# Performance work log

Measured on AMD Instinct MI355X. Metric: run time of the kernel, lower is better.

## Reference

```python
import jax, jax.numpy as jnp
import numpy as np

K = 7
TOWERS = 4
X_SIZE = 8
POS_SIZE = 3
NUM_GRAPHS = 128
NODES_PER_GRAPH = 512
N = NUM_GRAPHS * NODES_PER_GRAPH
EPS_STD = 1e-5  # PyG StdAggregation eps
BN_EPS = 1e-5
# degree histogram passed to PNAConv.__init__ -> avg log-degree used by scalers
_DEG_HIST = np.array([0, 0, 0, 0, 0, 100, 200, 700], dtype=np.float64)
_BINS = np.arange(_DEG_HIST.shape[0], dtype=np.float64)
AVG_DEG_LOG = float((np.log(_BINS + 1.0) * _DEG_HIST).sum() / _DEG_HIST.sum())


def knn_graph(pos, num_graphs, k):
    # batched kNN (loop=False): each node gets its k nearest neighbors within its graph
    Nn, D = pos.shape
    n = Nn // num_graphs
    p = pos.reshape(num_graphs, n, D)
    d2 = jnp.sum((p[:, :, None, :] - p[:, None, :, :]) ** 2, axis=-1)  # [B,n,n]
    d2 = d2 + jnp.eye(n, dtype=d2.dtype) * 1e10  # exclude self-loops
    _, idx = jax.lax.top_k(-d2, k)  # [B,n,k] local neighbor ids
    offs = (jnp.arange(num_graphs) * n)[:, None, None]
    return (idx + offs).reshape(Nn, k)  # global source ids per target node


def pna_conv(x, nbr, W_pre, b_pre, W_post, b_post, W_lin, b_lin):
    # PyG PNAConv, towers=4, pre_layers=1, post_layers=1, divide_input=False, edge_dim=None
    Nn, F = x.shape
    k = nbr.shape[1]
    x_j = x[nbr]                                              # gather sources [N,k,F]
    x_i = jnp.broadcast_to(x[:, None, :], (Nn, k, F))         # target features
    h = jnp.concatenate([x_i, x_j], axis=-1)                  # [N,k,2F]
    m = jnp.einsum('nke,tef->nktf', h, W_pre) + b_pre         # per-tower pre-MLP [N,k,T,F]
    mean = m.mean(axis=1)
    mn = m.min(axis=1)
    mx = m.max(axis=1)
    var = jnp.mean(m * m, axis=1) - mean * mean               # PyG VarAggregation
    std = jnp.sqrt(jax.nn.relu(var) + EPS_STD)
    agg = jnp.concatenate([mean, mn, mx, std], axis=-1)       # [N,T,4F]
    amp = jnp.log(k + 1.0) / AVG_DEG_LOG                      # deg == k for every node in a knn graph
    scaled = jnp.concatenate([agg, agg * amp, agg * (1.0 / amp)], axis=-1)  # identity/amp/atten [N,T,12F]
    out = jnp.concatenate([jnp.broadcast_to(x[:, None, :], (Nn, TOWERS, F)), scaled], axis=-1)  # [N,T,13F]
    out = jnp.einsum('ntg,tgf->ntf', out, W_post) + b_post    # per-tower post-MLP [N,T,F_out]
    out = out.reshape(Nn, -1)
    return out @ W_lin + b_lin                                # mixing Linear(out,out)


def batch_norm(x, g, b):
    # training-mode BatchNorm1d over the node dimension
    mu = x.mean(axis=0)
    var = x.var(axis=0)
    return g * (x - mu) * jax.lax.rsqrt(var + BN_EPS) + b


def forward(x, pos, W_pre1, b_pre1, W_post1, b_post1, W_lin1, b_lin1, bn1_g, bn1_b,
            W_pre2, b_pre2, W_post2, b_post2, W_lin2, b_lin2, bn2_g, bn2_b, num_graphs):
    nbr = knn_graph(pos, num_graphs, K)
    h = jax.nn.relu(batch_norm(pna_conv(x, nbr, W_pre1, b_pre1, W_post1, b_post1, W_lin1, b_lin1), bn1_g, bn1_b))
    h = jax.nn.relu(batch_norm(pna_conv(h, nbr, W_pre2, b_pre2, W_post2, b_post2, W_lin2, b_lin2), bn2_g, bn2_b))
    return h.reshape(num_graphs, -1, h.shape[-1]).mean(axis=1)  # global mean pool -> [B,128]


def _winit(key, shape):
    fan_in = shape[-2]
    return (jax.random.normal(key, shape, dtype=jnp.float32) / jnp.sqrt(jnp.float32(fan_in))).astype(jnp.float32)


def setup_inputs() -> dict:
    key = jax.random.key(0)
    ks = jax.random.split(key, 8)
    F1, F2 = X_SIZE, 64
    return {
        'x': jax.random.normal(ks[0], (N, X_SIZE), dtype=jnp.float32),
        'pos': jax.random.normal(ks[1], (N, POS_SIZE), dtype=jnp.float32),
        'W_pre1': _winit(ks[2], (TOWERS, 2 * F1, F1)),
        'b_pre1': jnp.zeros((TOWERS, F1), jnp.float32),
        'W_post1': _winit(ks[3], (TOWERS, 13 * F1, 64 // TOWERS)),
        'b_post1': jnp.zeros((TOWERS, 64 // TOWERS), jnp.float32),
        'W_lin1': _winit(ks[4], (64, 64)),
        'b_lin1': jnp.zeros((64,), jnp.float32),
        'bn1_g': jnp.ones((64,), jnp.float32),
        'bn1_b': jnp.zeros((64,), jnp.float32),
        'W_pre2': _winit(ks[5], (TOWERS, 2 * F2, F2)),
        'b_pre2': jnp.zeros((TOWERS, F2), jnp.float32),
        'W_post2': _winit(ks[6], (TOWERS, 13 * F2, 128 // TOWERS)),
        'b_post2': jnp.zeros((TOWERS, 128 // TOWERS), jnp.float32),
        'W_lin2': _winit(ks[7], (128, 128)),
        'b_lin2': jnp.zeros((128,), jnp.float32),
        'bn2_g': jnp.ones((128,), jnp.float32),
        'bn2_b': jnp.zeros((128,), jnp.float32),
        'num_graphs': NUM_GRAPHS,
    }


def reference(x, pos, W_pre1, b_pre1, W_post1, b_post1, W_lin1, b_lin1, bn1_g, bn1_b,
              W_pre2, b_pre2, W_post2, b_post2, W_lin2, b_lin2, bn2_g, bn2_b, num_graphs):
    return forward(x, pos, W_pre1, b_pre1, W_post1, b_post1, W_lin1, b_lin1, bn1_g, bn1_b,
                   W_pre2, b_pre2, W_post2, b_post2, W_lin2, b_lin2, bn2_g, bn2_b, num_graphs)
```

## Files before the change

kernel.cpp:

```cpp
#include <hip/hip_runtime.h>
#include <math.h>


#define NGRAPH 128
#define NPG    512
#define NN     (NGRAPH*NPG)
#define KNB    7

constexpr double AVG_DEG_LOG_D = 2.0239670479173344;
constexpr double LOG8_D        = 2.0794415416798357;

typedef _Float16 f16x8 __attribute__((ext_vector_type(8)));
typedef _Float16 h2    __attribute__((ext_vector_type(2)));
typedef float    f32x4 __attribute__((ext_vector_type(4)));

__device__ __forceinline__ unsigned short f2h(float x) {
    _Float16 h = (_Float16)x;
    return __builtin_bit_cast(unsigned short, h);
}

__global__ __launch_bounds__(256) void prep_kernel(
    const float* __restrict__ Wpost1, const float* __restrict__ Wpost2,
    const float* __restrict__ Wpre2,  const float* __restrict__ Wlin2,
    const float* __restrict__ Wlin1,
    unsigned short* __restrict__ Wf1p, unsigned short* __restrict__ Wf1l,
    unsigned short* __restrict__ Wfv, unsigned short* __restrict__ Wfu,
    unsigned short* __restrict__ Wfp, unsigned short* __restrict__ Wfl)
{
    const float AMP = (float)(LOG8_D / AVG_DEG_LOG_D);
    const float ATT = (float)(AVG_DEG_LOG_D / LOG8_D);
    for (int i = blockIdx.x*256 + threadIdx.x; i < 90112; i += gridDim.x*256) {
        if (i < 4096) {
            int t = i >> 10, kk = (i >> 9) & 1, lane = (i >> 3) & 63, j = i & 7;
            int k = kk*32 + ((lane >> 4) << 3) + j;
            int col = lane & 15;
            float val;
            if (k < 8)       val = Wpost1[(t*104 + k)*16 + col];
            else if (k < 40) {
                int g2 = k - 8;
                val = Wpost1[(t*104 +  8 + g2)*16 + col]
                    + AMP*Wpost1[(t*104 + 40 + g2)*16 + col]
                    + ATT*Wpost1[(t*104 + 72 + g2)*16 + col];
            } else val = 0.f;
            Wf1p[i] = f2h(val);
        } else if (i < 8192) {
            int jj = i - 4096;
            int kk = jj >> 11, tile = (jj >> 9) & 3, lane = (jj >> 3) & 63, j = jj & 7;
            int k = kk*32 + ((lane >> 4) << 3) + j;
            int col = tile*16 + (lane & 15);
            Wf1l[jj] = f2h(Wlin1[k*64 + col]);
        } else if (i < 24576) {
            int jj = i - 8192;
            int kk = jj >> 13, ct = (jj >> 9) & 15, lane = (jj >> 3) & 63, jf = jj & 7;
            int k   = kk*32 + ((lane >> 4) << 3) + jf;
            int col = ct*16 + (lane & 15);
            int t = col >> 6, f = col & 63;
            Wfv[jj] = f2h(Wpre2[(t*128 + 64 + k)*64 + f]);
        } else if (i < 32768) {
            int jj = i - 24576;
            int t = jj >> 11, kk = (jj >> 10) & 1, c = (jj >> 9) & 1, lane = (jj >> 3) & 63, jf = jj & 7;
            int k   = kk*32 + ((lane >> 4) << 3) + jf;
            int col = c*16 + (lane & 15);
            float acc = 0.f;
            for (int f = 0; f < 64; ++f) {
                float wu = 0.f;
#pragma unroll
                for (int s = 0; s < 3; ++s) {
                    int g2 = s*64 + f;
                    wu += Wpost2[(t*832 +  64 + g2)*32 + col]
                        + AMP*Wpost2[(t*832 + 320 + g2)*32 + col]
                        + ATT*Wpost2[(t*832 + 576 + g2)*32 + col];
                }
                acc += Wpre2[(t*128 + k)*64 + f] * wu;
            }
            Wfu[jj] = f2h(acc);
        } else if (i < 73728) {
            int jj = i - 32768;
            int t = jj / 10240, r = jj % 10240;
            int kk = r / 1024, r2 = r % 1024;
            int c = r2 >> 9, lane = (r2 >> 3) & 63, jf = r2 & 7;
            int G   = kk*32 + ((lane >> 4) << 3) + jf;
            int col = c*16 + (lane & 15);
            float val;
            if (G < 64) val = Wpost2[(t*832 + G)*32 + col];
            else {
                int g2 = G - 64;
                val = Wpost2[(t*832 +  64 + g2)*32 + col]
                    + AMP*Wpost2[(t*832 + 320 + g2)*32 + col]
                    + ATT*Wpost2[(t*832 + 576 + g2)*32 + col];
            }
            Wfp[jj] = f2h(val);
        } else {
            int jj = i - 73728;
            int kk = jj / 4096, r = jj % 4096;
            int tile = r >> 9, lane = (r >> 3) & 63, jf = r & 7;
            int k   = kk*32 + ((lane >> 4) << 3) + jf;
            int col = tile*16 + (lane & 15);
            Wfl[jj] = f2h(Wlin2[k*128 + col]);
        }
    }
}

__global__ __launch_bounds__(256) void knn_part_kernel(const float* __restrict__ pos, float2* __restrict__ part)
{
    __shared__ float4 cposS[128];
    const int b = blockIdx.x;
    const int g = b >> 3, h = (b >> 2) & 1, q = b & 3;
    const int gb = g * NPG;
    const int cbase = q * 128;
    if (threadIdx.x < 128) {
        int j = cbase + threadIdx.x;
        cposS[threadIdx.x] = make_float4(pos[(gb+j)*3+0], pos[(gb+j)*3+1], pos[(gb+j)*3+2], 0.f);
    }
    __syncthreads();
    const int i = h*256 + threadIdx.x;
    const float px = pos[(gb+i)*3+0], py = pos[(gb+i)*3+1], pz = pos[(gb+i)*3+2];
    float bd[KNB]; int bi[KNB];
#pragma unroll
    for (int e = 0; e < KNB; ++e) { bd[e] = 3.0e38f; bi[e] = -1; }
#pragma unroll 4
    for (int j = 0; j < 128; ++j) {
        float4 pj = cposS[j];
        float dx = px - pj.x, dy = py - pj.y, dz = pz - pj.z;
        float d2 = __fadd_rn(__fadd_rn(__fmul_rn(dx,dx), __fmul_rn(dy,dy)), __fmul_rn(dz,dz));
        if (cbase + j == i) d2 = __builtin_inff();
        bool cmp[KNB];
#pragma unroll
        for (int e = 0; e < KNB; ++e) cmp[e] = d2 < bd[e];
#pragma unroll
        for (int e = KNB-1; e >= 1; --e) {
            bd[e] = cmp[e-1] ? bd[e-1] : (cmp[e] ? d2 : bd[e]);
            bi[e] = cmp[e-1] ? bi[e-1] : (cmp[e] ? cbase + j : bi[e]);
        }
        bd[0] = cmp[0] ? d2 : bd[0];
        bi[0] = cmp[0] ? cbase + j : bi[0];
    }
    float2* dst = &part[((size_t)(g*NPG + i)*4 + q)*KNB];
#pragma unroll
    for (int e = 0; e < KNB; ++e) dst[e] = make_float2(bd[e], __int_as_float(bi[e]));
}

__global__ __launch_bounds__(256) void knn_merge_kernel(const float2* __restrict__ part, int* __restrict__ nbr)
{
    const int n = blockIdx.x*256 + threadIdx.x;
    const float4* p4 = (const float4*)&part[(size_t)n*28];
    float bd[KNB]; int bi[KNB];
#pragma unroll
    for (int e = 0; e < KNB; ++e) { bd[e] = 3.0e38f; bi[e] = -1; }
#pragma unroll
    for (int m4 = 0; m4 < 14; ++m4) {
        float4 pr = p4[m4];
#pragma unroll
        for (int half = 0; half < 2; ++half) {
            float d2  = half ? pr.z : pr.x;
            int   idx = __float_as_int(half ? pr.w : pr.y);
            bool cmp[KNB];
#pragma unroll
            for (int e = 0; e < KNB; ++e) cmp[e] = d2 < bd[e];
#pragma unroll
            for (int e = KNB-1; e >= 1; --e) {
                bd[e] = cmp[e-1] ? bd[e-1] : (cmp[e] ? d2 : bd[e]);
                bi[e] = cmp[e-1] ? bi[e-1] : (cmp[e] ? idx : bi[e]);
            }
            bd[0] = cmp[0] ? d2 : bd[0];
            bi[0] = cmp[0] ? idx : bi[0];
        }
    }
    const int gb = n & ~(NPG-1);
#pragma unroll
    for (int e = 0; e < KNB; ++e) nbr[n*KNB + e] = gb + bi[e];
}

__global__ __launch_bounds__(256) void a1_kernel(
    const float* __restrict__ x, const float* __restrict__ Wpre1, const float* __restrict__ bpre1,
    float* __restrict__ u1, float* __restrict__ v1)
{
    __shared__ float wS[512];
    __shared__ float bS[32];
    const int tid = threadIdx.x;
    wS[tid] = Wpre1[tid]; wS[tid+256] = Wpre1[tid+256];
    if (tid < 32) bS[tid] = bpre1[tid];
    __syncthreads();
    const int n  = blockIdx.x*8 + (tid>>5);
    const int tf = tid & 31;
    const int t = tf >> 3, f = tf & 7;
    float u = bS[tf], v = 0.f;
#pragma unroll
    for (int e = 0; e < 8; ++e) {
        float xv = x[n*8+e];
        u += xv * wS[(t*16 + e)*8 + f];
        v += xv * wS[(t*16 + 8 + e)*8 + f];
    }
    u1[n*32+tf] = u;
    v1[n*32+tf] = v;
}

__global__ __launch_bounds__(256) void b1_kernel(
    const float* __restrict__ x, const int* __restrict__ nbr,
    const float* __restrict__ u1, const float* __restrict__ v1,
    const unsigned short* __restrict__ Wf1p, const unsigned short* __restrict__ Wf1l,
    float* __restrict__ y1)
{
    __shared__ int nbrsS[112];
    __shared__ __align__(16) unsigned short actS[64*72];
    __shared__ __align__(16) unsigned short postS[16*72];
    const int tid  = threadIdx.x;
    const int base = blockIdx.x * 16;
    if (tid < 112) nbrsS[tid] = nbr[base*7 + tid];
    for (int i = tid; i < 384; i += 256) {
        int r = i / 6, gq = i - 6*r;
        *(ushort4*)&actS[r*72 + 40 + gq*4] = make_ushort4(0,0,0,0);
    }
#pragma unroll
    for (int it = 0; it < 2; ++it) {
        int i = tid + it*256;
        int n = i >> 5, r2 = i & 31, t = r2 >> 3, f = r2 & 7;
        actS[(n*4 + t)*72 + f] = f2h(x[(base+n)*8 + f]);
    }
    __syncthreads();
    {
        const int n = tid >> 4, cp = tid & 15;
        const int tf0 = cp*2, t = tf0 >> 3, f0 = tf0 & 7;
        float2 uu = *(const float2*)&u1[(base+n)*32 + tf0];
        float s0=0.f,s1=0.f,q0=0.f,q1=0.f;
        float mn0=3e38f,mn1=3e38f,mx0=-3e38f,mx1=-3e38f;
#pragma unroll
        for (int e = 0; e < 7; ++e) {
            float2 vv = *(const float2*)&v1[nbrsS[n*7+e]*32 + tf0];
            s0 += vv.x; q0 += vv.x*vv.x; mn0 = fminf(mn0, vv.x); mx0 = fmaxf(mx0, vv.x);
            s1 += vv.y; q1 += vv.y*vv.y; mn1 = fminf(mn1, vv.y); mx1 = fmaxf(mx1, vv.y);
        }
        float me0 = s0*(1.f/7.f), me1 = s1*(1.f/7.f);
        float sd0 = sqrtf(fmaxf(q0*(1.f/7.f) - me0*me0, 0.f) + 1e-5f);
        float sd1 = sqrtf(fmaxf(q1*(1.f/7.f) - me1*me1, 0.f) + 1e-5f);
        const int row = (n*4 + t)*72;
        ushort2 w_;
        w_.x = f2h(uu.x + me0); w_.y = f2h(uu.y + me1); *(ushort2*)&actS[row +  8 + f0] = w_;
        w_.x = f2h(uu.x + mn0); w_.y = f2h(uu.y + mn1); *(ushort2*)&actS[row + 16 + f0] = w_;
        w_.x = f2h(uu.x + mx0); w_.y = f2h(uu.y + mx1); *(ushort2*)&actS[row + 24 + f0] = w_;
        w_.x = f2h(sd0);        w_.y = f2h(sd1);        *(ushort2*)&actS[row + 32 + f0] = w_;
    }
    __syncthreads();
    const int l = tid & 63, w = tid >> 6;
    const int lr = l & 15, lk = l >> 4;
    f32x4 acc = {0.f,0.f,0.f,0.f};
    {
        const f16x8* WB = (const f16x8*)Wf1p;
#pragma unroll
        for (int kk = 0; kk < 2; ++kk) {
            f16x8 a = *(const f16x8*)&actS[(lr*4 + w)*72 + kk*32 + lk*8];
            f16x8 b = WB[(w*2 + kk)*64 + l];
            acc = __builtin_amdgcn_mfma_f32_16x16x32_f16(a, b, acc, 0, 0, 0);
        }
    }
#pragma unroll
    for (int j = 0; j < 4; ++j)
        postS[(lk*4 + j)*72 + w*16 + lr] = f2h(acc[j]);
    __syncthreads();
    f32x4 d = {0.f,0.f,0.f,0.f};
    {
        const f16x8* WB = (const f16x8*)Wf1l;
#pragma unroll
        for (int kk = 0; kk < 2; ++kk) {
            f16x8 a = *(const f16x8*)&postS[lr*72 + kk*32 + lk*8];
            f16x8 b = WB[(kk*4 + w)*64 + l];
            d = __builtin_amdgcn_mfma_f32_16x16x32_f16(a, b, d, 0, 0, 0);
        }
    }
#pragma unroll
    for (int j = 0; j < 4; ++j)
        y1[(base + lk*4 + j)*64 + w*16 + lr] = d[j];
}

template<int C>
__global__ __launch_bounds__(256) void bn_stats_kernel(
    const float* __restrict__ y, float* __restrict__ Ps, float* __restrict__ Pq)
{
    constexpr int IT     = (NN/1024)*(C/4)/256;
    constexpr int GROUPS = C/4;
    constexpr int REPS   = 256/GROUPS;
    const int tid = threadIdx.x;
    const float4* y4 = (const float4*)y + (size_t)blockIdx.x*256*IT;
    float4 s = make_float4(0.f,0.f,0.f,0.f), q = make_float4(0.f,0.f,0.f,0.f);
#pragma unroll
    for (int it = 0; it < IT; ++it) {
        float4 v = y4[it*256 + tid];
        s.x += v.x; s.y += v.y; s.z += v.z; s.w += v.w;
        q.x += v.x*v.x; q.y += v.y*v.y; q.z += v.z*v.z; q.w += v.w*v.w;
    }
    __shared__ float4 sS[256], qS[256];
    sS[tid] = s; qS[tid] = q;
    __syncthreads();
#pragma unroll
    for (int step = REPS/2; step >= 1; step >>= 1) {
        if (tid < step*GROUPS) {
            float4 s2 = sS[tid + step*GROUPS], q2 = qS[tid + step*GROUPS];
            float4 ss = sS[tid], qq = qS[tid];
            ss.x += s2.x; ss.y += s2.y; ss.z += s2.z; ss.w += s2.w;
            qq.x += q2.x; qq.y += q2.y; qq.z += q2.z; qq.w += q2.w;
            sS[tid] = ss; qS[tid] = qq;
        }
        __syncthreads();
    }
    if (tid < GROUPS) {
        ((float4*)&Ps[(size_t)blockIdx.x*C])[tid] = sS[tid];
        ((float4*)&Pq[(size_t)blockIdx.x*C])[tid] = qS[tid];
    }
}

template<int C>
__global__ __launch_bounds__(C) void finA_kernel(
    const float* __restrict__ Ps, const float* __restrict__ Pq,
    float* __restrict__ As, float* __restrict__ Aq)
{
    const int c = threadIdx.x, b = blockIdx.x;
    float s = 0.f, q = 0.f;
#pragma unroll
    for (int i = 0; i < 16; ++i) {
        s += Ps[(b*16 + i)*C + c];
        q += Pq[(b*16 + i)*C + c];
    }
    As[b*C + c] = s;
    Aq[b*C + c] = q;
}

template<int C>
__global__ __launch_bounds__(C) void fin_kernel(
    const float* __restrict__ As, const float* __restrict__ Aq,
    const float* __restrict__ g, const float* __restrict__ b,
    float* __restrict__ scO, float* __restrict__ shO)
{
    const int c = threadIdx.x;
    float s = 0.f, q = 0.f;
#pragma unroll 8
    for (int i = 0; i < 64; ++i) { s += As[i*C + c]; q += Aq[i*C + c]; }
    const float inv = 1.f/(float)NN;
    float mu  = s*inv;
    float var = q*inv - mu*mu;
    float sc  = g[c]*rsqrtf(var + 1e-5f);
    scO[c] = sc;
    shO[c] = b[c] - mu*sc;
}

__global__ __launch_bounds__(256) void a2_kernel(
    const float* __restrict__ y1raw, const float* __restrict__ sc1, const float* __restrict__ sh1,
    const unsigned short* __restrict__ Wfv,
    unsigned short* __restrict__ v2)
{
    __shared__ __align__(16) unsigned short a1S[64*72];
    const int tid  = threadIdx.x;
    const int base = blockIdx.x * 64;
#pragma unroll
    for (int it = 0; it < 4; ++it) {
        int i = tid + it*256;
        float4 vv = ((const float4*)y1raw)[blockIdx.x*1024 + i];
        int n = i >> 4, c0 = (i & 15)*4;
        float c_[4] = {vv.x, vv.y, vv.z, vv.w};
#pragma unroll
        for (int j = 0; j < 4; ++j) {
            int c = c0 + j;
            a1S[n*72 + c] = f2h(fmaxf(c_[j]*sc1[c] + sh1[c], 0.f));
        }
    }
    __syncthreads();
    const int l = tid & 63, w = tid >> 6;
    const int lr = l & 15, lk = l >> 4;
    const f16x8 a0  = *(const f16x8*)&a1S[(w*16 + lr)*72 +      lk*8];
    const f16x8 a1f = *(const f16x8*)&a1S[(w*16 + lr)*72 + 32 + lk*8];
    const f16x8* WB = (const f16x8*)Wfv;
#pragma unroll 4
    for (int ct = 0; ct < 16; ++ct) {
        f32x4 acc = {0.f,0.f,0.f,0.f};
        f16x8 b0 = WB[ct*64 + l];
        f16x8 b1 = WB[(16 + ct)*64 + l];
        acc = __builtin_amdgcn_mfma_f32_16x16x32_f16(a0,  b0, acc, 0, 0, 0);
        acc = __builtin_amdgcn_mfma_f32_16x16x32_f16(a1f, b1, acc, 0, 0, 0);
        const int col = ct*16 + lr;
#pragma unroll
        for (int j = 0; j < 4; ++j)
            v2[(size_t)(base + w*16 + lk*4 + j)*256 + col] = f2h(acc[j]);
    }
}

__global__ __launch_bounds__(256) void b2_kernel(
    const int* __restrict__ nbr, const float* __restrict__ y1raw,
    const float* __restrict__ sc1, const float* __restrict__ sh1,
    const unsigned short* __restrict__ v2,
    const unsigned short* __restrict__ Wfu,
    const unsigned short* __restrict__ Wfp, const unsigned short* __restrict__ Wfl,
    float* __restrict__ y2)
{
    __shared__ int nbrsS[112];
    __shared__ __align__(16) unsigned short a1S[16*72];
    __shared__ __align__(16) unsigned short aggS[64*264];
    __shared__ __align__(16) unsigned short postS[16*136];

    const int tid = threadIdx.x;
    const int ob   = blockIdx.x;
    const int xcd  = ob & 7, slot = ob >> 3;
    const int gph  = ((slot >> 5) << 3) + xcd;
    const int sub  = slot & 31;
    const int base = gph*NPG + sub*16;

    if (tid < 112) nbrsS[tid] = nbr[base*7 + tid];
    for (int i = tid; i < 1024; i += 256) {
        int c = i & 63, n = i >> 6;
        float a = fmaxf(y1raw[base*64 + i]*sc1[c] + sh1[c], 0.f);
        a1S[n*72 + c] = f2h(a);
    }
    __syncthreads();
    {
        const int ns = tid >> 5, cg = tid & 31;
        const int t = cg >> 3, f0 = (cg & 7) * 8;
        const h2 inv7 = { (_Float16)(1.f/7.f), (_Float16)(1.f/7.f) };
#pragma unroll
        for (int it = 0; it < 2; ++it) {
            const int ln = it*8 + ns;
            h2 z = { (_Float16)0.f, (_Float16)0.f };
            h2 s[4]  = {z,z,z,z};
            h2 q[4]  = {z,z,z,z};
            h2 mn[4], mx[4];
#pragma unroll
            for (int p = 0; p < 4; ++p) {
                mn[p] = h2{ (_Float16)65504.f, (_Float16)65504.f };
                mx[p] = h2{ (_Float16)-65504.f, (_Float16)-65504.f };
            }
#pragma unroll
            for (int e = 0; e < 7; ++e) {
                uint4 vv = *(const uint4*)&v2[(size_t)nbrsS[ln*7+e]*256 + cg*8];
                unsigned vw[4] = {vv.x, vv.y, vv.z, vv.w};
#pragma unroll
                for (int p = 0; p < 4; ++p) {
                    h2 v = __builtin_bit_cast(h2, vw[p]);
                    s[p] += v;
                    q[p] += v*v;
                    mn[p] = __builtin_elementwise_min(mn[p], v);
                    mx[p] = __builtin_elementwise_max(mx[p], v);
                }
            }
            unsigned meW[4], mnW[4], mxW[4], sdW[4];
#pragma unroll
            for (int p = 0; p < 4; ++p) {
                h2 me = s[p]*inv7;
                float m0 = (float)me[0], m1 = (float)me[1];
                float sd0 = sqrtf(fmaxf(fmaf((float)q[p][0], 1.f/7.f, -m0*m0), 0.f) + 1e-5f);
                float sd1 = sqrtf(fmaxf(fmaf((float)q[p][1], 1.f/7.f, -m1*m1), 0.f) + 1e-5f);
                h2 sd = { (_Float16)sd0, (_Float16)sd1 };
                meW[p] = __builtin_bit_cast(unsigned, me);
                mnW[p] = __builtin_bit_cast(unsigned, mn[p]);
                mxW[p] = __builtin_bit_cast(unsigned, mx[p]);
                sdW[p] = __builtin_bit_cast(unsigned, sd);
            }
            const int ro = (t*16 + ln)*264 + f0;
            *(uint4*)&aggS[ro      ] = make_uint4(meW[0], meW[1], meW[2], meW[3]);
            *(uint4*)&aggS[ro +  64] = make_uint4(mnW[0], mnW[1], mnW[2], mnW[3]);
            *(uint4*)&aggS[ro + 128] = make_uint4(mxW[0], mxW[1], mxW[2], mxW[3]);
            *(uint4*)&aggS[ro + 192] = make_uint4(sdW[0], sdW[1], sdW[2], sdW[3]);
        }
    }
    __syncthreads();
    const int l = tid & 63, w = tid >> 6;
    const int lr = l & 15, lk = l >> 4;
    f32x4 acc0 = {0.f,0.f,0.f,0.f}, acc1 = {0.f,0.f,0.f,0.f};
    {
        const f16x8* WP = (const f16x8*)Wfp;
        const f16x8* WU = (const f16x8*)Wfu;
#pragma unroll
        for (int kk = 0; kk < 12; ++kk) {
            f16x8 a, b0, b1;
            if (kk < 2) {
                a  = *(const f16x8*)&a1S[lr*72 + kk*32 + lk*8];
                b0 = WP[((w*10 + kk)*2 + 0)*64 + l];
                b1 = WP[((w*10 + kk)*2 + 1)*64 + l];
            } else if (kk < 4) {
                a  = *(const f16x8*)&a1S[lr*72 + (kk-2)*32 + lk*8];
                b0 = WU[((w*2 + (kk-2))*2 + 0)*64 + l];
                b1 = WU[((w*2 + (kk-2))*2 + 1)*64 + l];
            } else {
                a  = *(const f16x8*)&aggS[(w*16 + lr)*264 + (kk-4)*32 + lk*8];
                b0 = WP[((w*10 + (kk-2))*2 + 0)*64 + l];
                b1 = WP[((w*10 + (kk-2))*2 + 1)*64 + l];
            }
            acc0 = __builtin_amdgcn_mfma_f32_16x16x32_f16(a, b0, acc0, 0, 0, 0);
            acc1 = __builtin_amdgcn_mfma_f32_16x16x32_f16(a, b1, acc1, 0, 0, 0);
        }
    }
#pragma unroll
    for (int j = 0; j < 4; ++j) {
        const int row = lk*4 + j;
        postS[row*136 + w*32 +      lr] = f2h(acc0[j]);
        postS[row*136 + w*32 + 16 + lr] = f2h(acc1[j]);
    }
    __syncthreads();
    f32x4 d0 = {0.f,0.f,0.f,0.f}, d1 = {0.f,0.f,0.f,0.f};
    {
        const f16x8* WB = (const f16x8*)Wfl;
#pragma unroll
        for (int kk = 0; kk < 4; ++kk) {
            f16x8 a = *(const f16x8*)&postS[lr*136 + kk*32 + lk*8];
            f16x8 b0 = WB[(kk*8 + 2*w + 0)*64 + l];
            f16x8 b1 = WB[(kk*8 + 2*w + 1)*64 + l];
            d0 = __builtin_amdgcn_mfma_f32_16x16x32_f16(a, b0, d0, 0, 0, 0);
            d1 = __builtin_amdgcn_mfma_f32_16x16x32_f16(a, b1, d1, 0, 0, 0);
        }
    }
#pragma unroll
    for (int j = 0; j < 4; ++j) {
        const int row = lk*4 + j;
        y2[(base + row)*128 + w*32 +      lr] = d0[j];
        y2[(base + row)*128 + w*32 + 16 + lr] = d1[j];
    }
}

__global__ __launch_bounds__(128) void pool_part_kernel(
    const float* __restrict__ y2, const float* __restrict__ sc2, const float* __restrict__ sh2,
    float* __restrict__ Pp)
{
    const int c = threadIdx.x;
    const int b = blockIdx.x;
    const float sc = sc2[c];
    const float sh = sh2[c];
    float acc = 0.f;
    const size_t base = (size_t)b*64*128 + c;
#pragma unroll 4
    for (int i = 0; i < 64; ++i)
        acc += fmaxf(y2[base + (size_t)i*128]*sc + sh, 0.f);
    Pp[b*128 + c] = acc;
}

__global__ __launch_bounds__(128) void pool_fin_kernel(
    const float* __restrict__ Pp, float* __restrict__ out)
{
    const int c = threadIdx.x, g = blockIdx.x;
    float acc = 0.f;
#pragma unroll
    for (int i = 0; i < 8; ++i) acc += Pp[(g*8 + i)*128 + c];
    out[g*128 + c] = acc * (1.f/(float)NPG);
}

extern "C" void kernel_launch(void* const* d_in, const int* in_sizes, int n_in,
                              void* d_out, int out_size, void* d_ws, size_t ws_size,
                              hipStream_t stream)
{
    const float* x      = (const float*)d_in[0];
    const float* pos    = (const float*)d_in[1];
    const float* Wpre1  = (const float*)d_in[2];
    const float* bpre1  = (const float*)d_in[3];
    const float* Wpost1 = (const float*)d_in[4];
    const float* bpost1 = (const float*)d_in[5];
    const float* Wlin1  = (const float*)d_in[6];
    const float* blin1  = (const float*)d_in[7];
    const float* bn1g   = (const float*)d_in[8];
    const float* bn1b   = (const float*)d_in[9];
    const float* Wpre2  = (const float*)d_in[10];
    const float* bpre2  = (const float*)d_in[11];
    const float* Wpost2 = (const float*)d_in[12];
    const float* bpost2 = (const float*)d_in[13];
    const float* Wlin2  = (const float*)d_in[14];
    const float* blin2  = (const float*)d_in[15];
    const float* bn2g   = (const float*)d_in[16];
    const float* bn2b   = (const float*)d_in[17];
    float* out = (float*)d_out;
    (void)bpost1; (void)blin1; (void)bpre2; (void)bpost2; (void)blin2;

    char* ws = (char*)d_ws;
    size_t off = 0;
    auto alloc = [&](size_t bytes) { void* p = ws + off; off += (bytes + 255) & ~(size_t)255; return p; };
    int*    nbr  = (int*)   alloc((size_t)NN*7*4);
    float2* part = (float2*)alloc((size_t)NN*28*8);
    float* u1    = (float*)alloc((size_t)NN*32*4);
    float* v1    = (float*)alloc((size_t)NN*32*4);
    float* y1    = (float*)alloc((size_t)NN*64*4);
    unsigned short* v2 = (unsigned short*)alloc((size_t)NN*256*2);
    float* y2    = (float*)alloc((size_t)NN*128*4);
    unsigned short* Wf1p = (unsigned short*)alloc(4096*2);
    unsigned short* Wf1l = (unsigned short*)alloc(4096*2);
    unsigned short* Wfv = (unsigned short*)alloc(16384*2);
    unsigned short* Wfu = (unsigned short*)alloc(8192*2);
    unsigned short* Wfp = (unsigned short*)alloc(40960*2);
    unsigned short* Wfl = (unsigned short*)alloc(16384*2);
    float* P1s   = (float*)alloc(1024*64*4);
    float* P1q   = (float*)alloc(1024*64*4);
    float* A1s   = (float*)alloc(64*64*4);
    float* A1q   = (float*)alloc(64*64*4);
    float* sc1   = (float*)alloc(64*4);
    float* sh1   = (float*)alloc(64*4);
    float* P2s   = (float*)alloc(1024*128*4);
    float* P2q   = (float*)alloc(1024*128*4);
    float* A2s   = (float*)alloc(64*128*4);
    float* A2q   = (float*)alloc(64*128*4);
    float* sc2   = (float*)alloc(128*4);
    float* sh2   = (float*)alloc(128*4);
    float* Pp    = (float*)alloc(1024*128*4);

    prep_kernel<<<128, 256, 0, stream>>>(Wpost1, Wpost2, Wpre2, Wlin2, Wlin1,
                                         Wf1p, Wf1l, Wfv, Wfu, Wfp, Wfl);
    knn_part_kernel<<<NGRAPH*8, 256, 0, stream>>>(pos, part);
    knn_merge_kernel<<<NN/256, 256, 0, stream>>>(part, nbr);
    a1_kernel<<<NN/8, 256, 0, stream>>>(x, Wpre1, bpre1, u1, v1);
    b1_kernel<<<NN/16, 256, 0, stream>>>(x, nbr, u1, v1, Wf1p, Wf1l, y1);
    bn_stats_kernel<64><<<1024, 256, 0, stream>>>(y1, P1s, P1q);
    finA_kernel<64><<<64, 64, 0, stream>>>(P1s, P1q, A1s, A1q);
    fin_kernel<64><<<1, 64, 0, stream>>>(A1s, A1q, bn1g, bn1b, sc1, sh1);
    a2_kernel<<<NN/64, 256, 0, stream>>>(y1, sc1, sh1, Wfv, v2);
    b2_kernel<<<NN/16, 256, 0, stream>>>(nbr, y1, sc1, sh1, v2, Wfu, Wfp, Wfl, y2);
    bn_stats_kernel<128><<<1024, 256, 0, stream>>>(y2, P2s, P2q);
    finA_kernel<128><<<64, 128, 0, stream>>>(P2s, P2q, A2s, A2q);
    fin_kernel<128><<<1, 128, 0, stream>>>(A2s, A2q, bn2g, bn2b, sc2, sh2);
    pool_part_kernel<<<1024, 128, 0, stream>>>(y2, sc2, sh2, Pp);
    pool_fin_kernel<<<NGRAPH, 128, 0, stream>>>(Pp, out);
}
```

Before: 174.5 us.

## Compute aggregation directly into MFMA A-fragment registers, dropping LDS staging

In b2_kernel, each lane now gathers and reduces the neighbor features that map exactly to its own MFMA A-operand slots (node lr, channels g0 and g0+32), so the aggregated mean/min/max/std values stay in registers as f16x8 fragments. This removes the 33 KB aggS shared buffer, its stores, and one __syncthreads. The cost is more registers per thread and a gather pattern where the 16 lanes sharing lk read different neighbor rows, which may reduce coalescing. The smaller LDS footprint could also allow more resident blocks per CU.

```diff
diff --git a/kernel.cpp b/kernel.cpp
--- a/kernel.cpp
+++ b/kernel.cpp
@@ -392,7 +392,6 @@
 {
     __shared__ int nbrsS[112];
     __shared__ __align__(16) unsigned short a1S[16*72];
-    __shared__ __align__(16) unsigned short aggS[64*264];
     __shared__ __align__(16) unsigned short postS[16*136];
 
     const int tid = threadIdx.x;
@@ -409,80 +408,96 @@
         a1S[n*72 + c] = f2h(a);
     }
     __syncthreads();
-    {
-        const int ns = tid >> 5, cg = tid & 31;
-        const int t = cg >> 3, f0 = (cg & 7) * 8;
-        const h2 inv7 = { (_Float16)(1.f/7.f), (_Float16)(1.f/7.f) };
-#pragma unroll
-        for (int it = 0; it < 2; ++it) {
-            const int ln = it*8 + ns;
-            h2 z = { (_Float16)0.f, (_Float16)0.f };
-            h2 s[4]  = {z,z,z,z};
-            h2 q[4]  = {z,z,z,z};
-            h2 mn[4], mx[4];
-#pragma unroll
-            for (int p = 0; p < 4; ++p) {
-                mn[p] = h2{ (_Float16)65504.f, (_Float16)65504.f };
-                mx[p] = h2{ (_Float16)-65504.f, (_Float16)-65504.f };
-            }
-#pragma unroll
-            for (int e = 0; e < 7; ++e) {
-                uint4 vv = *(const uint4*)&v2[(size_t)nbrsS[ln*7+e]*256 + cg*8];
-                unsigned vw[4] = {vv.x, vv.y, vv.z, vv.w};
-#pragma unroll
-                for (int p = 0; p < 4; ++p) {
-                    h2 v = __builtin_bit_cast(h2, vw[p]);
-                    s[p] += v;
-                    q[p] += v*v;
-                    mn[p] = __builtin_elementwise_min(mn[p], v);
-                    mx[p] = __builtin_elementwise_max(mx[p], v);
-                }
-            }
-            unsigned meW[4], mnW[4], mxW[4], sdW[4];
-#pragma unroll
-            for (int p = 0; p < 4; ++p) {
-                h2 me = s[p]*inv7;
-                float m0 = (float)me[0], m1 = (float)me[1];
-                float sd0 = sqrtf(fmaxf(fmaf((float)q[p][0], 1.f/7.f, -m0*m0), 0.f) + 1e-5f);
-                float sd1 = sqrtf(fmaxf(fmaf((float)q[p][1], 1.f/7.f, -m1*m1), 0.f) + 1e-5f);
-                h2 sd = { (_Float16)sd0, (_Float16)sd1 };
-                meW[p] = __builtin_bit_cast(unsigned, me);
-                mnW[p] = __builtin_bit_cast(unsigned, mn[p]);
-                mxW[p] = __builtin_bit_cast(unsigned, mx[p]);
-                sdW[p] = __builtin_bit_cast(unsigned, sd);
-            }
-            const int ro = (t*16 + ln)*264 + f0;
-            *(uint4*)&aggS[ro      ] = make_uint4(meW[0], meW[1], meW[2], meW[3]);
-            *(uint4*)&aggS[ro +  64] = make_uint4(mnW[0], mnW[1], mnW[2], mnW[3]);
-            *(uint4*)&aggS[ro + 128] = make_uint4(mxW[0], mxW[1], mxW[2], mxW[3]);
-            *(uint4*)&aggS[ro + 192] = make_uint4(sdW[0], sdW[1], sdW[2], sdW[3]);
-        }
-    }
-    __syncthreads();
     const int l = tid & 63, w = tid >> 6;
     const int lr = l & 15, lk = l >> 4;
+    const int g0 = w*64 + lk*8;
+    const int g1 = g0 + 32;
+    const h2 inv7 = { (_Float16)(1.f/7.f), (_Float16)(1.f/7.f) };
+    h2 z = { (_Float16)0.f, (_Float16)0.f };
+    h2 sA[4] = {z,z,z,z}, qA[4] = {z,z,z,z};
+    h2 sB[4] = {z,z,z,z}, qB[4] = {z,z,z,z};
+    h2 mnA[4], mxA[4], mnB[4], mxB[4];
+#pragma unroll
+    for (int p = 0; p < 4; ++p) {
+        mnA[p] = h2{ (_Float16)65504.f, (_Float16)65504.f };  mnB[p] = mnA[p];
+        mxA[p] = h2{ (_Float16)-65504.f, (_Float16)-65504.f }; mxB[p] = mxA[p];
+    }
+#pragma unroll
+    for (int e = 0; e < 7; ++e) {
+        const size_t nb = (size_t)nbrsS[lr*7 + e] * 256;
+        uint4 va = *(const uint4*)&v2[nb + g0];
+        uint4 vb = *(const uint4*)&v2[nb + g1];
+        unsigned aw[4] = {va.x, va.y, va.z, va.w};
+        unsigned bw[4] = {vb.x, vb.y, vb.z, vb.w};
+#pragma unroll
+        for (int p = 0; p < 4; ++p) {
+            h2 v = __builtin_bit_cast(h2, aw[p]);
+            sA[p] += v; qA[p] += v*v;
+            mnA[p] = __builtin_elementwise_min(mnA[p], v);
+            mxA[p] = __builtin_elementwise_max(mxA[p], v);
+            h2 u = __builtin_bit_cast(h2, bw[p]);
+            sB[p] += u; qB[p] += u*u;
+            mnB[p] = __builtin_elementwise_min(mnB[p], u);
+            mxB[p] = __builtin_elementwise_max(mxB[p], u);
+        }
+    }
+    unsigned meAW[4], sdAW[4], meBW[4], sdBW[4];
+#pragma unroll
+    for (int p = 0; p < 4; ++p) {
+        h2 meA = sA[p]*inv7;
+        h2 meB = sB[p]*inv7;
+        float a0 = (float)meA[0], a1v = (float)meA[1];
+        float b0 = (float)meB[0], b1v = (float)meB[1];
+        float sa0 = sqrtf(fmaxf(fmaf((float)qA[p][0], 1.f/7.f, -a0*a0), 0.f) + 1e-5f);
+        float sa1 = sqrtf(fmaxf(fmaf((float)qA[p][1], 1.f/7.f, -a1v*a1v), 0.f) + 1e-5f);
+        float sb0 = sqrtf(fmaxf(fmaf((float)qB[p][0], 1.f/7.f, -b0*b0), 0.f) + 1e-5f);
+        float sb1 = sqrtf(fmaxf(fmaf((float)qB[p][1], 1.f/7.f, -b1v*b1v), 0.f) + 1e-5f);
+        h2 sdA = { (_Float16)sa0, (_Float16)sa1 };
+        h2 sdB = { (_Float16)sb0, (_Float16)sb1 };
+        meAW[p] = __builtin_bit_cast(unsigned, meA);
+        meBW[p] = __builtin_bit_cast(unsigned, meB);
+        sdAW[p] = __builtin_bit_cast(unsigned, sdA);
+        sdBW[p] = __builtin_bit_cast(unsigned, sdB);
+    }
+    f16x8 fr[8];
+    fr[0] = __builtin_bit_cast(f16x8, make_uint4(meAW[0], meAW[1], meAW[2], meAW[3]));
+    fr[1] = __builtin_bit_cast(f16x8, make_uint4(meBW[0], meBW[1], meBW[2], meBW[3]));
+    fr[2] = __builtin_bit_cast(f16x8, make_uint4(__builtin_bit_cast(unsigned, mnA[0]), __builtin_bit_cast(unsigned, mnA[1]),
+                                                 __builtin_bit_cast(unsigned, mnA[2]), __builtin_bit_cast(unsigned, mnA[3])));
+    fr[3] = __builtin_bit_cast(f16x8, make_uint4(__builtin_bit_cast(unsigned, mnB[0]), __builtin_bit_cast(unsigned, mnB[1]),
+                                                 __builtin_bit_cast(unsigned, mnB[2]), __builtin_bit_cast(unsigned, mnB[3])));
+    fr[4] = __builtin_bit_cast(f16x8, make_uint4(__builtin_bit_cast(unsigned, mxA[0]), __builtin_bit_cast(unsigned, mxA[1]),
+                                                 __builtin_bit_cast(unsigned, mxA[2]), __builtin_bit_cast(unsigned, mxA[3])));
+    fr[5] = __builtin_bit_cast(f16x8, make_uint4(__builtin_bit_cast(unsigned, mxB[0]), __builtin_bit_cast(unsigned, mxB[1]),
+                                                 __builtin_bit_cast(unsigned, mxB[2]), __builtin_bit_cast(unsigned, mxB[3])));
+    fr[6] = __builtin_bit_cast(f16x8, make_uint4(sdAW[0], sdAW[1], sdAW[2], sdAW[3]));
+    fr[7] = __builtin_bit_cast(f16x8, make_uint4(sdBW[0], sdBW[1], sdBW[2], sdBW[3]));
     f32x4 acc0 = {0.f,0.f,0.f,0.f}, acc1 = {0.f,0.f,0.f,0.f};
     {
         const f16x8* WP = (const f16x8*)Wfp;
         const f16x8* WU = (const f16x8*)Wfu;
 #pragma unroll
-        for (int kk = 0; kk < 12; ++kk) {
-            f16x8 a, b0, b1;
-            if (kk < 2) {
-                a  = *(const f16x8*)&a1S[lr*72 + kk*32 + lk*8];
-                b0 = WP[((w*10 + kk)*2 + 0)*64 + l];
-                b1 = WP[((w*10 + kk)*2 + 1)*64 + l];
-            } else if (kk < 4) {
-                a  = *(const f16x8*)&a1S[lr*72 + (kk-2)*32 + lk*8];
-                b0 = WU[((w*2 + (kk-2))*2 + 0)*64 + l];
-                b1 = WU[((w*2 + (kk-2))*2 + 1)*64 + l];
-            } else {
-                a  = *(const f16x8*)&aggS[(w*16 + lr)*264 + (kk-4)*32 + lk*8];
-                b0 = WP[((w*10 + (kk-2))*2 + 0)*64 + l];
-                b1 = WP[((w*10 + (kk-2))*2 + 1)*64 + l];
-            }
+        for (int kk = 0; kk < 2; ++kk) {
+            f16x8 a = *(const f16x8*)&a1S[lr*72 + kk*32 + lk*8];
+            f16x8 b0 = WP[((w*10 + kk)*2 + 0)*64 + l];
+            f16x8 b1 = WP[((w*10 + kk)*2 + 1)*64 + l];
             acc0 = __builtin_amdgcn_mfma_f32_16x16x32_f16(a, b0, acc0, 0, 0, 0);
             acc1 = __builtin_amdgcn_mfma_f32_16x16x32_f16(a, b1, acc1, 0, 0, 0);
+        }
+#pragma unroll
+        for (int kk = 0; kk < 2; ++kk) {
+            f16x8 a = *(const f16x8*)&a1S[lr*72 + kk*32 + lk*8];
+            f16x8 b0 = WU[((w*2 + kk)*2 + 0)*64 + l];
+            f16x8 b1 = WU[((w*2 + kk)*2 + 1)*64 + l];
+            acc0 = __builtin_amdgcn_mfma_f32_16x16x32_f16(a, b0, acc0, 0, 0, 0);
+            acc1 = __builtin_amdgcn_mfma_f32_16x16x32_f16(a, b1, acc1, 0, 0, 0);
+        }
+#pragma unroll
+        for (int c = 0; c < 8; ++c) {
+            f16x8 b0 = WP[((w*10 + c + 2)*2 + 0)*64 + l];
+            f16x8 b1 = WP[((w*10 + c + 2)*2 + 1)*64 + l];
+            acc0 = __builtin_amdgcn_mfma_f32_16x16x32_f16(fr[c], b0, acc0, 0, 0, 0);
+            acc1 = __builtin_amdgcn_mfma_f32_16x16x32_f16(fr[c], b1, acc1, 0, 0, 0);
         }
     }
 #pragma unroll
```

After: 184.2 us. +5.6%, slower.
